# Kernel optimization log

Measured on AMD Instinct MI355X. Metric: run time of the kernel, lower is better.

The kernel has to match this reference:

```python
import jax, jax.numpy as jnp
import numpy as np
import math

B, S, D, H = 2, 2048, 1024, 16
DK = D // H


def setup_inputs() -> dict:
    key = jax.random.key(0)
    ks = jax.random.split(key, 14)
    inp = {
        "query": jax.random.normal(ks[0], (B, S, D), dtype=jnp.float32),
        "key": jax.random.normal(ks[1], (B, S, D), dtype=jnp.float32),
        "value": jax.random.normal(ks[2], (B, S, D), dtype=jnp.float32),
        "group_prob": jax.random.uniform(ks[3], (B, S, S), dtype=jnp.float32),
        "mask": jax.random.randint(ks[4], (B, S), 0, 2, dtype=jnp.int32),
    }
    scale = 0.02
    inp["Wq"] = jax.random.normal(ks[5], (D, D), dtype=jnp.float32) * scale
    inp["bq"] = jnp.zeros((D,), dtype=jnp.float32)
    inp["Wk"] = jax.random.normal(ks[6], (D, D), dtype=jnp.float32) * scale
    inp["bk"] = jnp.zeros((D,), dtype=jnp.float32)
    inp["Wv"] = jax.random.normal(ks[7], (D, D), dtype=jnp.float32) * scale
    inp["bv"] = jnp.zeros((D,), dtype=jnp.float32)
    inp["Wo"] = jax.random.normal(ks[8], (D, D), dtype=jnp.float32) * scale
    inp["bo"] = jnp.zeros((D,), dtype=jnp.float32)
    return inp


def reference(query, key, value, group_prob, mask, Wq, bq, Wk, bk, Wv, bv, Wo, bo):
    b, s, d = query.shape
    # project and split heads: [B,S,D] -> [B,H,S,DK]
    def proj(x, W, bias):
        return (x @ W.T + bias).reshape(b, s, H, DK).transpose(0, 2, 1, 3)

    q = proj(query, Wq, bq)
    k = proj(key, Wk, bk)
    v = proj(value, Wv, bv)

    scores = jnp.einsum("bhqd,bhkd->bhqk", q, k) / math.sqrt(DK)  # [B,H,S,S]

    # combined mask: padding-row mask OR diagonal (always attend to self)
    eye = jnp.eye(s, dtype=jnp.int32)
    combined = mask[:, None, None, :] | eye[None, None, :, :]  # [B,1,S,S]
    scores = jnp.where(combined == 0, jnp.float32(-1e9), scores)

    p_attn = jax.nn.softmax(scores, axis=-1)
    p_attn = p_attn * group_prob[:, None, :, :]  # post-softmax group scaling

    x = jnp.einsum("bhqk,bhkd->bhqd", p_attn, v)  # [B,H,S,DK]
    x = x.transpose(0, 2, 1, 3).reshape(b, s, d)
    return x @ Wo.T + bo
```

## Files before the change

### kernel.cpp

```cpp
#include <hip/hip_runtime.h>
#include <hip/hip_bf16.h>
#include <stdint.h>

typedef __bf16 bf16x8 __attribute__((ext_vector_type(8)));
typedef float f32x4 __attribute__((ext_vector_type(4)));

#define QSCALE 0.1803368801111244f

__device__ __forceinline__ void gld16(const void* g, void* l) {
  __builtin_amdgcn_global_load_lds(
      (__attribute__((address_space(1))) void*)(uintptr_t)(g),
      (__attribute__((address_space(3))) void*)(l), 16, 0, 0);
}

struct CastArgs {
  const float* src[7];
  __bf16* dst[7];
  int n[7];
};

__global__ __launch_bounds__(256) void cast_bf16_kernel(CastArgs a) {
  const int t = blockIdx.y;
  const int i = (blockIdx.x * 256 + threadIdx.x) * 8;
  if (i >= a.n[t]) return;
  const float4* s = (const float4*)(a.src[t] + i);
  float4 v0 = s[0], v1 = s[1];
  bf16x8 o;
  o[0] = (__bf16)v0.x; o[1] = (__bf16)v0.y; o[2] = (__bf16)v0.z; o[3] = (__bf16)v0.w;
  o[4] = (__bf16)v1.x; o[5] = (__bf16)v1.y; o[6] = (__bf16)v1.z; o[7] = (__bf16)v1.w;
  *(bf16x8*)(a.dst[t] + i) = o;
}

struct QkvArgs {
  const __bf16* A[3];
  const __bf16* B[3];
  const float* bias[3];
  __bf16* out[3];
};

__global__ __launch_bounds__(512) void qkv_gemm(QkvArgs args) {
  __shared__ __align__(16) __bf16 As[128 * 32];
  __shared__ __align__(16) __bf16 Bs[128 * 32];
  const int tid = threadIdx.x;
  const int z = blockIdx.y;
  const int bx = blockIdx.x;
  const int m0 = (z < 2 ? (bx >> 3) : (bx & 7)) * 128;
  const int n0 = (z < 2 ? (bx & 7) : (bx >> 3)) * 128;
  const __bf16* A = args.A[z];
  const __bf16* B = args.B[z];
  const float* bias = args.bias[z];
  __bf16* out = args.out[z];
  const float scale = (z == 0) ? QSCALE : 1.0f;

  const int lane = tid & 63, wid = tid >> 6;
  const int wm = (wid & 3) * 32, wn = (wid >> 2) * 64;
  const int l16 = lane & 15, quad = lane >> 4;

  const int sc = (tid & 3) ^ ((tid >> 2) & 3);
  const __bf16* ga = A + (size_t)(m0 + (tid >> 2)) * 1024 + sc * 8;
  const __bf16* gb = B + (size_t)(n0 + (tid >> 2)) * 1024 + sc * 8;
  char* lA = (char*)As + tid * 16;
  char* lB = (char*)Bs + tid * 16;
  const int a_off = (wm + l16) * 64 + ((quad ^ (l16 & 3)) * 16);
  const int b_off = (wn + l16) * 64 + ((quad ^ (l16 & 3)) * 16);

  f32x4 acc[2][4] = {};

  for (int k0 = 0; k0 < 1024; k0 += 32) {
    __syncthreads();
    gld16(ga + k0, lA);
    gld16(gb + k0, lB);
    __syncthreads();
    bf16x8 af[2], bfr[4];
#pragma unroll
    for (int mi = 0; mi < 2; ++mi)
      af[mi] = *(const bf16x8*)((const char*)As + a_off + mi * 1024);
#pragma unroll
    for (int ni = 0; ni < 4; ++ni)
      bfr[ni] = *(const bf16x8*)((const char*)Bs + b_off + ni * 1024);
#pragma unroll
    for (int mi = 0; mi < 2; ++mi)
#pragma unroll
      for (int ni = 0; ni < 4; ++ni)
        acc[mi][ni] = __builtin_amdgcn_mfma_f32_16x16x32_bf16(af[mi], bfr[ni],
                                                              acc[mi][ni], 0, 0, 0);
  }

  if (z < 2) {
#pragma unroll
    for (int ni = 0; ni < 4; ++ni) {
      const int col = n0 + wn + ni * 16 + l16;
      const int h = col >> 6, dk = col & 63;
      const float bb = bias[col];
#pragma unroll
      for (int mi = 0; mi < 2; ++mi)
#pragma unroll
        for (int r = 0; r < 4; ++r) {
          const int row = m0 + wm + mi * 16 + quad * 4 + r;
          const int b = row >> 11, s = row & 2047;
          out[((size_t)(b * 16 + h) * 2048 + s) * 64 + dk] =
              (__bf16)((acc[mi][ni][r] + bb) * scale);
        }
    }
  } else {
#pragma unroll
    for (int mi = 0; mi < 2; ++mi)
#pragma unroll
      for (int r = 0; r < 4; ++r) {
        const int rowm = m0 + wm + mi * 16 + quad * 4 + r;
        const int h = rowm >> 6, dk = rowm & 63;
        const float bb = bias[rowm];
#pragma unroll
        for (int ni = 0; ni < 4; ++ni) {
          const int coln = n0 + wn + ni * 16 + l16;
          const int b = coln >> 11, s = coln & 2047;
          out[((size_t)(b * 16 + h) * 64 + dk) * 2048 + s] =
              (__bf16)(acc[mi][ni][r] + bb);
        }
      }
  }
}

__global__ __launch_bounds__(512) void gemm_out(const __bf16* __restrict__ A,
                                                const __bf16* __restrict__ B,
                                                const float* __restrict__ bias,
                                                float* __restrict__ out) {
  __shared__ __align__(16) __bf16 As[128 * 32];
  __shared__ __align__(16) __bf16 Bs[128 * 32];
  const int tid = threadIdx.x;
  const int m0 = blockIdx.y * 128;
  const int n0 = blockIdx.x * 128;
  const int lane = tid & 63, wid = tid >> 6;
  const int wm = (wid & 3) * 32, wn = (wid >> 2) * 64;
  const int l16 = lane & 15, quad = lane >> 4;

  const int sc = (tid & 3) ^ ((tid >> 2) & 3);
  const __bf16* ga = A + (size_t)(m0 + (tid >> 2)) * 1024 + sc * 8;
  const __bf16* gb = B + (size_t)(n0 + (tid >> 2)) * 1024 + sc * 8;
  char* lA = (char*)As + tid * 16;
  char* lB = (char*)Bs + tid * 16;
  const int a_off = (wm + l16) * 64 + ((quad ^ (l16 & 3)) * 16);
  const int b_off = (wn + l16) * 64 + ((quad ^ (l16 & 3)) * 16);

  f32x4 acc[2][4] = {};

  for (int k0 = 0; k0 < 1024; k0 += 32) {
    __syncthreads();
    gld16(ga + k0, lA);
    gld16(gb + k0, lB);
    __syncthreads();
    bf16x8 af[2], bfr[4];
#pragma unroll
    for (int mi = 0; mi < 2; ++mi)
      af[mi] = *(const bf16x8*)((const char*)As + a_off + mi * 1024);
#pragma unroll
    for (int ni = 0; ni < 4; ++ni)
      bfr[ni] = *(const bf16x8*)((const char*)Bs + b_off + ni * 1024);
#pragma unroll
    for (int mi = 0; mi < 2; ++mi)
#pragma unroll
      for (int ni = 0; ni < 4; ++ni)
        acc[mi][ni] = __builtin_amdgcn_mfma_f32_16x16x32_bf16(af[mi], bfr[ni],
                                                              acc[mi][ni], 0, 0, 0);
  }

#pragma unroll
  for (int ni = 0; ni < 4; ++ni) {
    const int col = n0 + wn + ni * 16 + l16;
    const float bb = bias[col];
#pragma unroll
    for (int mi = 0; mi < 2; ++mi)
#pragma unroll
      for (int r = 0; r < 4; ++r) {
        const int row = m0 + wm + mi * 16 + quad * 4 + r;
        out[(size_t)row * 1024 + col] = acc[mi][ni][r] + bb;
      }
  }
}

__global__ __launch_bounds__(512, 4) void attn_kernel(
    const __bf16* __restrict__ Qh, const __bf16* __restrict__ Kh,
    const __bf16* __restrict__ Vt, const float* __restrict__ gprob,
    const int* __restrict__ maskp, __bf16* __restrict__ xb) {
  __shared__ __align__(16) __bf16 Ks[2][64 * 64];
  __shared__ __align__(16) __bf16 Vs[2][64 * 64];
  __shared__ unsigned long long mbits[32];

  const int tid = threadIdx.x;
  const int qt = blockIdx.x, bh = blockIdx.y;
  const int b = bh >> 4, h = bh & 15;
  const int q0 = qt * 128;
  const int lane = tid & 63, wid = tid >> 6, l16 = lane & 15, quad = lane >> 4;
  const size_t head_off = (size_t)bh * (2048 * 64);

  const int srow = tid >> 3;
  const int sc8 = (tid & 7) ^ (srow & 7);
  const int fxor = (l16 & 7);

  const int sig = ((srow & 16) << 1) + ((srow & 12) << 1) + ((srow & 32) >> 3) +
                  (srow & 3);

  const __bf16* gk0 = Kh + head_off + (size_t)sig * 64 + sc8 * 8;
  const __bf16* gv0 = Vt + head_off + (size_t)srow * 2048 + sc8 * 8;

  gld16(gk0, (char*)Ks + tid * 16);
  gld16(gv0, (char*)Vs + tid * 16);

  bf16x8 aq[2];
  {
    const __bf16* gq = Qh + head_off + (size_t)(q0 + wid * 16 + l16) * 64 + quad * 8;
    aq[0] = *(const bf16x8*)(gq);
    aq[1] = *(const bf16x8*)(gq + 32);
  }

  int irow[4];
#pragma unroll
  for (int r = 0; r < 4; ++r) irow[r] = q0 + wid * 16 + quad * 4 + r;

  const float* gpl = gprob + (size_t)b * 2048 * 2048 +
                     (size_t)(q0 + wid * 16 + l16) * 2048 + quad * 8;
  float4 g0 = *(const float4*)(gpl);
  float4 g1 = *(const float4*)(gpl + 4);
  float4 g2 = *(const float4*)(gpl + 32);
  float4 g3 = *(const float4*)(gpl + 36);

  {
    const int* mr = maskp + b * 2048;
#pragma unroll
    for (int t = 0; t < 4; ++t) {
      const int kt2 = wid * 4 + t;
      const int mv = mr[kt2 * 64 + lane];
      const unsigned long long bal = __ballot(mv != 0);
      if (lane == 0) mbits[kt2] = bal;
    }
  }
  __syncthreads();

  f32x4 o[4] = {};
  float lp = 0.f;

  const int dkt = qt * 2 + (wid >> 2);
  const int kqbase = (wid & 3) * 16 + l16 - quad * 8;

  for (int kt = 0; kt < 32; ++kt) {
    const int cur = kt & 1;
    float4 gn0, gn1, gn2, gn3;
    if (kt < 31) {
      const int nb = cur ^ 1;
      gld16(gk0 + (kt + 1) * 4096, (char*)Ks + nb * 8192 + tid * 16);
      gld16(gv0 + (kt + 1) * 64, (char*)Vs + nb * 8192 + tid * 16);
      const float* gn = gpl + (kt + 1) * 64;
      gn0 = *(const float4*)(gn);
      gn1 = *(const float4*)(gn + 4);
      gn2 = *(const float4*)(gn + 32);
      gn3 = *(const float4*)(gn + 36);
    }

    const unsigned long long sh = mbits[kt] >> (quad * 8);
    const uint32_t shlo = (uint32_t)sh, shhi = (uint32_t)(sh >> 32);

    f32x4 p2[4] = {};
#pragma unroll
    for (int kh = 0; kh < 2; ++kh)
#pragma unroll
      for (int ni = 0; ni < 4; ++ni) {
        bf16x8 bk = *(const bf16x8*)((const char*)Ks + cur * 8192 +
                                     (ni * 16 + l16) * 128 +
                                     (((kh * 4 + quad) ^ fxor) * 16));
        p2[ni] = __builtin_amdgcn_mfma_f32_16x16x32_bf16(bk, aq[kh], p2[ni], 0, 0, 0);
      }

    const float gfl[16] = {g0.x, g0.y, g0.z, g0.w, g1.x, g1.y, g1.z, g1.w,
                           g2.x, g2.y, g2.z, g2.w, g3.x, g3.y, g3.z, g3.w};
    bf16x8 pa0, pa1;
    if (kt != dkt) {
#pragma unroll
      for (int ni = 0; ni < 4; ++ni)
#pragma unroll
        for (int r = 0; r < 4; ++r) {
          const int j = ((ni >> 1) << 2) + r;
          const float e = __builtin_exp2f(p2[ni][r]);
          const bool mk = (((ni & 1) ? shhi : shlo) >> j) & 1;
          const float em = mk ? e : 0.f;
          lp += em;
          const float pg = em * gfl[(ni & 1) * 8 + j];
          if (ni & 1) pa1[j] = (__bf16)pg; else pa0[j] = (__bf16)pg;
        }
    } else {
#pragma unroll
      for (int ni = 0; ni < 4; ++ni)
#pragma unroll
        for (int r = 0; r < 4; ++r) {
          const int j = ((ni >> 1) << 2) + r;
          const float e = __builtin_exp2f(p2[ni][r]);
          const bool mk = (((ni & 1) ? shhi : shlo) >> j) & 1;
          const bool diag = (kqbase == ((ni & 1) * 32 + j));
          const float em = (mk || diag) ? e : 0.f;
          lp += em;
          const float pg = em * gfl[(ni & 1) * 8 + j];
          if (ni & 1) pa1[j] = (__bf16)pg; else pa0[j] = (__bf16)pg;
        }
    }

#pragma unroll
    for (int kh = 0; kh < 2; ++kh) {
      const bf16x8 pa = kh ? pa1 : pa0;
#pragma unroll
      for (int ni = 0; ni < 4; ++ni) {
        bf16x8 bv = *(const bf16x8*)((const char*)Vs + cur * 8192 +
                                     (ni * 16 + l16) * 128 +
                                     (((kh * 4 + quad) ^ fxor) * 16));
        o[ni] = __builtin_amdgcn_mfma_f32_16x16x32_bf16(pa, bv, o[ni], 0, 0, 0);
      }
    }

    if (kt < 31) { g0 = gn0; g1 = gn1; g2 = gn2; g3 = gn3; }
    __syncthreads();
  }

  lp += __shfl_xor(lp, 16);
  lp += __shfl_xor(lp, 32);
  float rinv[4];
#pragma unroll
  for (int r = 0; r < 4; ++r) rinv[r] = 1.f / __shfl(lp, quad * 4 + r);
#pragma unroll
  for (int ni = 0; ni < 4; ++ni) {
    const int dk = ni * 16 + l16;
#pragma unroll
    for (int r = 0; r < 4; ++r) {
      const float val = o[ni][r] * rinv[r];
      xb[((size_t)(b * 2048 + irow[r])) * 1024 + h * 64 + dk] = (__bf16)val;
    }
  }
}

extern "C" void kernel_launch(void* const* d_in, const int* in_sizes, int n_in,
                              void* d_out, int out_size, void* d_ws, size_t ws_size,
                              hipStream_t stream) {
  const float* query = (const float*)d_in[0];
  const float* key_  = (const float*)d_in[1];
  const float* value = (const float*)d_in[2];
  const float* gprob = (const float*)d_in[3];
  const int*   maskp = (const int*)d_in[4];
  const float* Wq = (const float*)d_in[5];
  const float* bq = (const float*)d_in[6];
  const float* Wk = (const float*)d_in[7];
  const float* bk = (const float*)d_in[8];
  const float* Wv = (const float*)d_in[9];
  const float* bv = (const float*)d_in[10];
  const float* Wo = (const float*)d_in[11];
  const float* bo = (const float*)d_in[12];

  char* ws = (char*)d_ws;
  const size_t MB = 1 << 20;
  __bf16* qb  = (__bf16*)(ws + 0 * MB);
  __bf16* kb  = (__bf16*)(ws + 8 * MB);
  __bf16* vb  = (__bf16*)(ws + 16 * MB);
  __bf16* Wqb = (__bf16*)(ws + 24 * MB);
  __bf16* Wkb = (__bf16*)(ws + 26 * MB);
  __bf16* Wvb = (__bf16*)(ws + 28 * MB);
  __bf16* Wob = (__bf16*)(ws + 30 * MB);
  __bf16* Qh  = (__bf16*)(ws + 32 * MB);
  __bf16* Kh  = (__bf16*)(ws + 40 * MB);
  __bf16* Vt  = (__bf16*)(ws + 48 * MB);
  __bf16* xb  = (__bf16*)(ws + 56 * MB);

  CastArgs ca;
  ca.src[0] = query; ca.dst[0] = qb;  ca.n[0] = 4194304;
  ca.src[1] = key_;  ca.dst[1] = kb;  ca.n[1] = 4194304;
  ca.src[2] = value; ca.dst[2] = vb;  ca.n[2] = 4194304;
  ca.src[3] = Wq;    ca.dst[3] = Wqb; ca.n[3] = 1048576;
  ca.src[4] = Wk;    ca.dst[4] = Wkb; ca.n[4] = 1048576;
  ca.src[5] = Wv;    ca.dst[5] = Wvb; ca.n[5] = 1048576;
  ca.src[6] = Wo;    ca.dst[6] = Wob; ca.n[6] = 1048576;
  cast_bf16_kernel<<<dim3(2048, 7), 256, 0, stream>>>(ca);

  QkvArgs qa;
  qa.A[0] = qb;  qa.B[0] = Wqb; qa.bias[0] = bq; qa.out[0] = Qh;
  qa.A[1] = kb;  qa.B[1] = Wkb; qa.bias[1] = bk; qa.out[1] = Kh;
  qa.A[2] = Wvb; qa.B[2] = vb;  qa.bias[2] = bv; qa.out[2] = Vt;
  qkv_gemm<<<dim3(256, 3), 512, 0, stream>>>(qa);

  attn_kernel<<<dim3(16, 32), 512, 0, stream>>>(Qh, Kh, Vt, gprob, maskp, xb);
  gemm_out<<<dim3(8, 32), 512, 0, stream>>>(xb, Wob, bo, (float*)d_out);
}
```

Measured before the change: 286.4 us.

## Split key tiles across two wave groups per attention block with LDS reduction

The attention block grows to 1024 threads, split into two 512-thread groups. Each group processes half of the 32 key/value tiles with its own double-buffered LDS region, and the partial output accumulators and row sums are combined through LDS at the end. This doubles the waves working on each query tile to hide load and exp latency. The cost is a final reduction, more LDS per block, and register pressure under the tighter launch bounds.

After: 659.7 us. 2.3x slower.

```diff
diff --git a/kernel.cpp b/kernel.cpp
--- a/kernel.cpp
+++ b/kernel.cpp
@@ -178,23 +178,26 @@
   }
 }
 
-__global__ __launch_bounds__(512, 4) void attn_kernel(
+__global__ __launch_bounds__(1024, 8) void attn_kernel(
     const __bf16* __restrict__ Qh, const __bf16* __restrict__ Kh,
     const __bf16* __restrict__ Vt, const float* __restrict__ gprob,
     const int* __restrict__ maskp, __bf16* __restrict__ xb) {
-  __shared__ __align__(16) __bf16 Ks[2][64 * 64];
-  __shared__ __align__(16) __bf16 Vs[2][64 * 64];
+  __shared__ __align__(16) __bf16 Ks[2][2][64 * 64];
+  __shared__ __align__(16) __bf16 Vs[2][2][64 * 64];
   __shared__ unsigned long long mbits[32];
 
   const int tid = threadIdx.x;
   const int qt = blockIdx.x, bh = blockIdx.y;
   const int b = bh >> 4, h = bh & 15;
   const int q0 = qt * 128;
-  const int lane = tid & 63, wid = tid >> 6, l16 = lane & 15, quad = lane >> 4;
+  const int lane = tid & 63, wid = tid >> 6;
+  const int wg = wid & 7, grp = wid >> 3;
+  const int l16 = lane & 15, quad = lane >> 4;
   const size_t head_off = (size_t)bh * (2048 * 64);
 
-  const int srow = tid >> 3;
-  const int sc8 = (tid & 7) ^ (srow & 7);
+  const int gtid = tid & 511;
+  const int srow = gtid >> 3;
+  const int sc8 = (gtid & 7) ^ (srow & 7);
   const int fxor = (l16 & 7);
 
   const int sig = ((srow & 16) << 1) + ((srow & 12) << 1) + ((srow & 32) >> 3) +
@@ -202,33 +205,31 @@
 
   const __bf16* gk0 = Kh + head_off + (size_t)sig * 64 + sc8 * 8;
   const __bf16* gv0 = Vt + head_off + (size_t)srow * 2048 + sc8 * 8;
-
-  gld16(gk0, (char*)Ks + tid * 16);
-  gld16(gv0, (char*)Vs + tid * 16);
+  char* ksg = (char*)Ks + grp * 16384;
+  char* vsg = (char*)Vs + grp * 16384;
+
+  gld16(gk0 + (size_t)(grp * 16) * 4096, ksg + gtid * 16);
+  gld16(gv0 + (grp * 16) * 64, vsg + gtid * 16);
 
   bf16x8 aq[2];
   {
-    const __bf16* gq = Qh + head_off + (size_t)(q0 + wid * 16 + l16) * 64 + quad * 8;
+    const __bf16* gq = Qh + head_off + (size_t)(q0 + wg * 16 + l16) * 64 + quad * 8;
     aq[0] = *(const bf16x8*)(gq);
     aq[1] = *(const bf16x8*)(gq + 32);
   }
 
-  int irow[4];
-#pragma unroll
-  for (int r = 0; r < 4; ++r) irow[r] = q0 + wid * 16 + quad * 4 + r;
-
   const float* gpl = gprob + (size_t)b * 2048 * 2048 +
-                     (size_t)(q0 + wid * 16 + l16) * 2048 + quad * 8;
-  float4 g0 = *(const float4*)(gpl);
-  float4 g1 = *(const float4*)(gpl + 4);
-  float4 g2 = *(const float4*)(gpl + 32);
-  float4 g3 = *(const float4*)(gpl + 36);
+                     (size_t)(q0 + wg * 16 + l16) * 2048 + quad * 8;
+  float4 g0 = *(const float4*)(gpl + grp * 1024);
+  float4 g1 = *(const float4*)(gpl + grp * 1024 + 4);
+  float4 g2 = *(const float4*)(gpl + grp * 1024 + 32);
+  float4 g3 = *(const float4*)(gpl + grp * 1024 + 36);
 
   {
     const int* mr = maskp + b * 2048;
 #pragma unroll
-    for (int t = 0; t < 4; ++t) {
-      const int kt2 = wid * 4 + t;
+    for (int t = 0; t < 2; ++t) {
+      const int kt2 = wid * 2 + t;
       const int mv = mr[kt2 * 64 + lane];
       const unsigned long long bal = __ballot(mv != 0);
       if (lane == 0) mbits[kt2] = bal;
@@ -239,17 +240,18 @@
   f32x4 o[4] = {};
   float lp = 0.f;
 
-  const int dkt = qt * 2 + (wid >> 2);
-  const int kqbase = (wid & 3) * 16 + l16 - quad * 8;
-
-  for (int kt = 0; kt < 32; ++kt) {
-    const int cur = kt & 1;
+  const int dkt = qt * 2 + (wg >> 2);
+  const int kqbase = (wg & 3) * 16 + l16 - quad * 8;
+
+  for (int i = 0; i < 16; ++i) {
+    const int kt = grp * 16 + i;
+    const int cur = i & 1;
     float4 gn0, gn1, gn2, gn3;
-    if (kt < 31) {
+    if (i < 15) {
       const int nb = cur ^ 1;
-      gld16(gk0 + (kt + 1) * 4096, (char*)Ks + nb * 8192 + tid * 16);
-      gld16(gv0 + (kt + 1) * 64, (char*)Vs + nb * 8192 + tid * 16);
-      const float* gn = gpl + (kt + 1) * 64;
+      gld16(gk0 + (size_t)(kt + 1) * 4096, ksg + nb * 8192 + gtid * 16);
+      gld16(gv0 + (kt + 1) * 64, vsg + nb * 8192 + gtid * 16);
+      const float* gn = gpl + (size_t)(kt + 1) * 64;
       gn0 = *(const float4*)(gn);
       gn1 = *(const float4*)(gn + 4);
       gn2 = *(const float4*)(gn + 32);
@@ -264,8 +266,7 @@
     for (int kh = 0; kh < 2; ++kh)
 #pragma unroll
       for (int ni = 0; ni < 4; ++ni) {
-        bf16x8 bk = *(const bf16x8*)((const char*)Ks + cur * 8192 +
-                                     (ni * 16 + l16) * 128 +
+        bf16x8 bk = *(const bf16x8*)(ksg + cur * 8192 + (ni * 16 + l16) * 128 +
                                      (((kh * 4 + quad) ^ fxor) * 16));
         p2[ni] = __builtin_amdgcn_mfma_f32_16x16x32_bf16(bk, aq[kh], p2[ni], 0, 0, 0);
       }
@@ -307,29 +308,52 @@
       const bf16x8 pa = kh ? pa1 : pa0;
 #pragma unroll
       for (int ni = 0; ni < 4; ++ni) {
-        bf16x8 bv = *(const bf16x8*)((const char*)Vs + cur * 8192 +
-                                     (ni * 16 + l16) * 128 +
+        bf16x8 bv = *(const bf16x8*)(vsg + cur * 8192 + (ni * 16 + l16) * 128 +
                                      (((kh * 4 + quad) ^ fxor) * 16));
         o[ni] = __builtin_amdgcn_mfma_f32_16x16x32_bf16(pa, bv, o[ni], 0, 0, 0);
       }
     }
 
-    if (kt < 31) { g0 = gn0; g1 = gn1; g2 = gn2; g3 = gn3; }
+    if (i < 15) { g0 = gn0; g1 = gn1; g2 = gn2; g3 = gn3; }
     __syncthreads();
   }
 
-  lp += __shfl_xor(lp, 16);
-  lp += __shfl_xor(lp, 32);
-  float rinv[4];
-#pragma unroll
-  for (int r = 0; r < 4; ++r) rinv[r] = 1.f / __shfl(lp, quad * 4 + r);
-#pragma unroll
-  for (int ni = 0; ni < 4; ++ni) {
-    const int dk = ni * 16 + l16;
-#pragma unroll
-    for (int r = 0; r < 4; ++r) {
-      const float val = o[ni][r] * rinv[r];
-      xb[((size_t)(b * 2048 + irow[r])) * 1024 + h * 64 + dk] = (__bf16)val;
+  float* po = (float*)(&Ks[0][0][0]);
+  float* pl = (float*)(&Vs[0][0][0]);
+  const int cidx = wg * 64 + lane;
+  if (grp == 1) {
+#pragma unroll
+    for (int ni = 0; ni < 4; ++ni)
+#pragma unroll
+      for (int r = 0; r < 4; ++r)
+        po[(ni * 4 + r) * 512 + cidx] = o[ni][r];
+    pl[cidx] = lp;
+  }
+  __syncthreads();
+  if (grp == 0) {
+#pragma unroll
+    for (int ni = 0; ni < 4; ++ni)
+#pragma unroll
+      for (int r = 0; r < 4; ++r)
+        o[ni][r] += po[(ni * 4 + r) * 512 + cidx];
+    lp += pl[cidx];
+
+    lp += __shfl_xor(lp, 16);
+    lp += __shfl_xor(lp, 32);
+    float rinv[4];
+#pragma unroll
+    for (int r = 0; r < 4; ++r) rinv[r] = 1.f / __shfl(lp, quad * 4 + r);
+    int irow[4];
+#pragma unroll
+    for (int r = 0; r < 4; ++r) irow[r] = q0 + wg * 16 + quad * 4 + r;
+#pragma unroll
+    for (int ni = 0; ni < 4; ++ni) {
+      const int dk = ni * 16 + l16;
+#pragma unroll
+      for (int r = 0; r < 4; ++r) {
+        const float val = o[ni][r] * rinv[r];
+        xb[((size_t)(b * 2048 + irow[r])) * 1024 + h * 64 + dk] = (__bf16)val;
+      }
     }
   }
 }
@@ -381,6 +405,6 @@
   qa.A[2] = Wvb; qa.B[2] = vb;  qa.bias[2] = bv; qa.out[2] = Vt;
   qkv_gemm<<<dim3(256, 3), 512, 0, stream>>>(qa);
 
-  attn_kernel<<<dim3(16, 32), 512, 0, stream>>>(Qh, Kh, Vt, gprob, maskp, xb);
+  attn_kernel<<<dim3(16, 32), 1024, 0, stream>>>(Qh, Kh, Vt, gprob, maskp, xb);
   gemm_out<<<dim3(8, 32), 512, 0, stream>>>(xb, Wob, bo, (float*)d_out);
 }
```
